# Performance work log

Hardware: AMD Instinct MI355X
Metric: run time of the kernel (lower is better)

Reference implementation:

```python
import jax, jax.numpy as jnp
import numpy as np

DIM = 768
HEADS = 12
HEAD_DIM = DIM // HEADS
HIDDEN = int(DIM * 4.0)
EPS = 1e-5


def _layernorm(x, g, b):
    mu = jnp.mean(x, axis=-1, keepdims=True)
    var = jnp.mean(jnp.square(x - mu), axis=-1, keepdims=True)
    return (x - mu) * jax.lax.rsqrt(var + EPS) * g + b


def setup_inputs() -> dict:
    key = jax.random.key(0)
    ks = jax.random.split(key, 8)
    s_in = 1.0 / np.sqrt(DIM)
    s_hid = 1.0 / np.sqrt(HIDDEN)
    return {
        "x": jax.random.normal(ks[0], (2, 2048, DIM), dtype=jnp.float32),
        "ln1_g": jnp.ones((DIM,), jnp.float32),
        "ln1_b": jnp.zeros((DIM,), jnp.float32),
        "w_qkv": jax.random.normal(ks[1], (DIM, 3 * DIM), jnp.float32) * s_in,
        "w_proj": jax.random.normal(ks[2], (DIM, DIM), jnp.float32) * s_in,
        "b_proj": jnp.zeros((DIM,), jnp.float32),
        "ln2_g": jnp.ones((DIM,), jnp.float32),
        "ln2_b": jnp.zeros((DIM,), jnp.float32),
        "w_fc1": jax.random.normal(ks[3], (DIM, HIDDEN), jnp.float32) * s_in,
        "b_fc1": jnp.zeros((HIDDEN,), jnp.float32),
        "w_fc2": jax.random.normal(ks[4], (HIDDEN, DIM), jnp.float32) * s_hid,
        "b_fc2": jnp.zeros((DIM,), jnp.float32),
    }


def reference(x, ln1_g, ln1_b, w_qkv, w_proj, b_proj, ln2_g, ln2_b, w_fc1, b_fc1, w_fc2, b_fc2):
    b, n, c = x.shape
    scale = HEAD_DIM ** -0.5

    # --- attention branch ---
    h = _layernorm(x, ln1_g, ln1_b)
    qkv = (h @ w_qkv).reshape(b, n, 3, HEADS, HEAD_DIM)
    q, k, v = jnp.moveaxis(qkv, 2, 0)          # each [b, n, H, hd]
    attn = jnp.einsum("bqhd,bkhd->bhqk", q, k) * scale
    attn = jax.nn.softmax(attn, axis=-1)       # [b, H, n, n] (naive, materialized)
    o = jnp.einsum("bhqk,bkhd->bqhd", attn, v).reshape(b, n, c)
    x = x + o @ w_proj + b_proj

    # --- MLP branch ---
    h2 = _layernorm(x, ln2_g, ln2_b)
    m = jax.nn.gelu(h2 @ w_fc1 + b_fc1, approximate=False)
    x = x + m @ w_fc2 + b_fc2
    return x
```

## Files before the change

### kernel.cpp

```cpp
#include <hip/hip_runtime.h>
#include <math.h>


typedef unsigned short u16;
typedef __attribute__((ext_vector_type(8))) short short8;
typedef __attribute__((ext_vector_type(4))) float f32x4;

#define TOKENS 4096
#define DIM    768
#define QKV_N  2304
#define HID    3072
#define NSEQ   2048
#define NHEAD  12
#define HDIM   64

__device__ __forceinline__ float bf2f(u16 u) {
  union { unsigned i; float f; } v; v.i = ((unsigned)u) << 16; return v.f;
}
__device__ __forceinline__ u16 f2bf(float f) {
  union { float f; unsigned i; } v; v.f = f;
  unsigned r = v.i + 0x7fffu + ((v.i >> 16) & 1u);
  return (u16)(r >> 16);
}
__device__ __forceinline__ unsigned pack_bf2(float a, float b) {
  union { float f; unsigned i; } x, y; x.f = a; y.f = b;
  return (x.i >> 16) | (y.i & 0xffff0000u);
}
__device__ __forceinline__ void pl32swap(unsigned &a, unsigned &b) {
  asm("v_permlane32_swap_b32 %0, %1" : "+v"(a), "+v"(b));
}
__device__ __forceinline__ void pl16swap(unsigned &a, unsigned &b) {
  asm("v_permlane16_swap_b32 %0, %1" : "+v"(a), "+v"(b));
}

__device__ __forceinline__ void async_copy16(const u16* g, u16* l) {
  __builtin_amdgcn_global_load_lds(
      (const __attribute__((address_space(1))) unsigned int*)(unsigned long long)g,
      (__attribute__((address_space(3))) unsigned int*)(unsigned int)(unsigned long long)l,
      16, 0, 0);
}

__global__ __launch_bounds__(256) void prep_kernel(
    const float* __restrict__ x, const float* __restrict__ g,
    const float* __restrict__ b, u16* __restrict__ h,
    const float* __restrict__ in0, u16* __restrict__ out0,
    const float* __restrict__ in1, u16* __restrict__ out1,
    const float* __restrict__ in2, u16* __restrict__ out2,
    const float* __restrict__ in3, u16* __restrict__ out3) {
  const int tid = threadIdx.x;
  if (blockIdx.x < 1024) {
    int wave = tid >> 6, lane = tid & 63;
    int token = blockIdx.x * 4 + wave;
    float v[12];
    const float4* xr = (const float4*)(x + (size_t)token * DIM);
#pragma unroll
    for (int w = 0; w < 3; w++) {
      float4 q = xr[lane + w * 64];
      v[w * 4 + 0] = q.x; v[w * 4 + 1] = q.y; v[w * 4 + 2] = q.z; v[w * 4 + 3] = q.w;
    }
    float s = 0.f;
#pragma unroll
    for (int i = 0; i < 12; i++) s += v[i];
#pragma unroll
    for (int off = 32; off > 0; off >>= 1) s += __shfl_xor(s, off);
    float mu = s * (1.0f / DIM);
    float ss = 0.f;
#pragma unroll
    for (int i = 0; i < 12; i++) { float d = v[i] - mu; ss += d * d; }
#pragma unroll
    for (int off = 32; off > 0; off >>= 1) ss += __shfl_xor(ss, off);
    float rs = rsqrtf(ss * (1.0f / DIM) + 1e-5f);
    ushort4* orow = (ushort4*)(h + (size_t)token * DIM);
    const float4* g4 = (const float4*)g;
    const float4* b4 = (const float4*)b;
#pragma unroll
    for (int w = 0; w < 3; w++) {
      float4 gq = g4[lane + w * 64], bq = b4[lane + w * 64];
      ushort4 o;
      o.x = f2bf((v[w * 4 + 0] - mu) * rs * gq.x + bq.x);
      o.y = f2bf((v[w * 4 + 1] - mu) * rs * gq.y + bq.y);
      o.z = f2bf((v[w * 4 + 2] - mu) * rs * gq.z + bq.z);
      o.w = f2bf((v[w * 4 + 3] - mu) * rs * gq.w + bq.w);
      orow[lane + w * 64] = o;
    }
    return;
  }
  __shared__ u16 t[32][33];
  int bid = blockIdx.x - 1024, rem;
  const float* in; u16* out; int R, C;
  if (bid < 1728)      { in = in0; out = out0; R = 768;  C = 2304; rem = bid; }
  else if (bid < 2304) { in = in1; out = out1; R = 768;  C = 768;  rem = bid - 1728; }
  else if (bid < 4608) { in = in2; out = out2; R = 768;  C = 3072; rem = bid - 2304; }
  else                 { in = in3; out = out3; R = 3072; C = 768;  rem = bid - 4608; }
  int c0 = (rem % (C / 32)) * 32, r0 = (rem / (C / 32)) * 32;
  int tx = tid & 31, ty = tid >> 5;
#pragma unroll
  for (int i = 0; i < 4; i++)
    t[ty + i * 8][tx] = f2bf(in[(size_t)(r0 + ty + i * 8) * C + c0 + tx]);
  __syncthreads();
#pragma unroll
  for (int i = 0; i < 4; i++)
    out[(size_t)(c0 + ty + i * 8) * R + r0 + tx] = t[tx][ty + i * 8];
}

__global__ __launch_bounds__(256) void ln_kernel(const u16* __restrict__ xin,
                                                 const float* __restrict__ g,
                                                 const float* __restrict__ b,
                                                 u16* __restrict__ out) {
  int wave = threadIdx.x >> 6, lane = threadIdx.x & 63;
  int token = blockIdx.x * 4 + wave;
  float v[12];
  const ushort4* xr = (const ushort4*)(xin + (size_t)token * DIM);
#pragma unroll
  for (int w = 0; w < 3; w++) {
    ushort4 q = xr[lane + w * 64];
    v[w * 4 + 0] = bf2f(q.x); v[w * 4 + 1] = bf2f(q.y);
    v[w * 4 + 2] = bf2f(q.z); v[w * 4 + 3] = bf2f(q.w);
  }
  float s = 0.f;
#pragma unroll
  for (int i = 0; i < 12; i++) s += v[i];
#pragma unroll
  for (int off = 32; off > 0; off >>= 1) s += __shfl_xor(s, off);
  float mu = s * (1.0f / DIM);
  float ss = 0.f;
#pragma unroll
  for (int i = 0; i < 12; i++) { float d = v[i] - mu; ss += d * d; }
#pragma unroll
  for (int off = 32; off > 0; off >>= 1) ss += __shfl_xor(ss, off);
  float rs = rsqrtf(ss * (1.0f / DIM) + 1e-5f);

  ushort4* orow = (ushort4*)(out + (size_t)token * DIM);
  const float4* g4 = (const float4*)g;
  const float4* b4 = (const float4*)b;
#pragma unroll
  for (int w = 0; w < 3; w++) {
    float4 gq = g4[lane + w * 64], bq = b4[lane + w * 64];
    ushort4 o;
    o.x = f2bf((v[w * 4 + 0] - mu) * rs * gq.x + bq.x);
    o.y = f2bf((v[w * 4 + 1] - mu) * rs * gq.y + bq.y);
    o.z = f2bf((v[w * 4 + 2] - mu) * rs * gq.z + bq.z);
    o.w = f2bf((v[w * 4 + 3] - mu) * rs * gq.w + bq.w);
    orow[lane + w * 64] = o;
  }
}

template <int BM, int BN, int EPI>
__global__ __launch_bounds__(256, 3) void gemm_bt(
    const u16* __restrict__ A, const u16* __restrict__ BT,
    void* __restrict__ Cout, const float* __restrict__ bias,
    const void* __restrict__ resid, int M, int N, int K,
    u16* __restrict__ vtb) {
  constexpr int MT = BM / 32, NT = BN / 32;
  constexpr int ACH = BM / 16;
  constexpr int CPW = (BM + BN) / 64;
  __shared__ __align__(16) u16 Alds[2][BM * 32];
  __shared__ __align__(16) u16 Blds[2][BN * 32];
  const int tid = threadIdx.x;
  const int lane = tid & 63, wave = tid >> 6;
  const int wr = wave >> 1, wc = wave & 1;
  const int nby = M / BM;
  const int by = blockIdx.x % nby, bx = blockIdx.x / nby;
  const int bm = by * BM, bn = bx * BN;
  const int c16 = lane & 15, quad = lane >> 4;
  const int l4 = lane >> 2;
  const int lc = (((lane & 3) ^ ((l4 >> 1) & 3)) * 8);
  const int fsw = (c16 >> 1) & 3;

  f32x4 acc[MT][NT];
#pragma unroll
  for (int i = 0; i < MT; i++)
#pragma unroll
    for (int j = 0; j < NT; j++) acc[i][j] = (f32x4){0.f, 0.f, 0.f, 0.f};

  const u16* gsrc[CPW];
  u16* ldst[CPW];
  int hstep[CPW];
#pragma unroll
  for (int c = 0; c < CPW; c++) {
    int chunk = wave * CPW + c;
    if (chunk < ACH) {
      gsrc[c] = A + (size_t)(bm + chunk * 16 + l4) * K + lc;
      ldst[c] = Alds[0] + chunk * 512;
      hstep[c] = BM * 32;
    } else {
      int bc = chunk - ACH;
      gsrc[c] = BT + (size_t)(bn + bc * 16 + l4) * K + lc;
      ldst[c] = Blds[0] + bc * 512;
      hstep[c] = BN * 32;
    }
  }

  for (int kk = 0; kk < K; kk += 64) {
    __syncthreads();
#pragma unroll
    for (int c = 0; c < CPW; c++) {
      async_copy16(gsrc[c] + kk, ldst[c]);
      async_copy16(gsrc[c] + kk + 32, ldst[c] + hstep[c]);
    }
    __syncthreads();
#pragma unroll
    for (int ks = 0; ks < 2; ks++) {
      short8 af[MT], bfr[NT];
#pragma unroll
      for (int mt = 0; mt < MT; mt++)
        af[mt] = *(const short8*)(Alds[ks] + (wr * (BM / 2) + mt * 16 + c16) * 32 +
                                  ((quad ^ fsw)) * 8);
#pragma unroll
      for (int nt = 0; nt < NT; nt++)
        bfr[nt] = *(const short8*)(Blds[ks] + (wc * (BN / 2) + nt * 16 + c16) * 32 +
                                   ((quad ^ fsw)) * 8);
#pragma unroll
      for (int mt = 0; mt < MT; mt++)
#pragma unroll
        for (int nt = 0; nt < NT; nt++)
          acc[mt][nt] = __builtin_amdgcn_mfma_f32_16x16x32_bf16(af[mt], bfr[nt],
                                                                acc[mt][nt], 0, 0, 0);
    }
  }

#pragma unroll
  for (int mt = 0; mt < MT; mt++) {
#pragma unroll
    for (int nt = 0; nt < NT; nt++) {
      int col = bn + wc * (BN / 2) + nt * 16 + c16;
      float bv = (EPI != 0) ? bias[col] : 0.f;
      int row0 = bm + wr * (BM / 2) + mt * 16 + quad * 4;
      if (EPI == 0 && col >= 2 * DIM) {
        int b = row0 >> 11;
        ushort4 pk;
        pk.x = f2bf(acc[mt][nt][0]); pk.y = f2bf(acc[mt][nt][1]);
        pk.z = f2bf(acc[mt][nt][2]); pk.w = f2bf(acc[mt][nt][3]);
        *(ushort4*)(vtb + ((size_t)b * DIM + col - 2 * DIM) * NSEQ + (row0 & 2047)) = pk;
        continue;
      }
#pragma unroll
      for (int r = 0; r < 4; r++) {
        int row = row0 + r;
        float vv = acc[mt][nt][r];
        if (EPI == 1) {
          vv += bv + ((const float*)resid)[(size_t)row * N + col];
          ((u16*)Cout)[(size_t)row * N + col] = f2bf(vv);
        } else if (EPI == 2) {
          vv += bv;
          vv = 0.5f * vv * (1.0f + erff(vv * 0.70710678118654752f));
          ((u16*)Cout)[(size_t)row * N + col] = f2bf(vv);
        } else if (EPI == 3) {
          vv += bv + bf2f(((const u16*)resid)[(size_t)row * N + col]);
          ((float*)Cout)[(size_t)row * N + col] = vv;
        } else {
          ((u16*)Cout)[(size_t)row * N + col] = f2bf(vv);
        }
      }
    }
  }
}

__global__ __launch_bounds__(256, 3) void attn_kernel(const u16* __restrict__ qkv,
                                                      const u16* __restrict__ vt,
                                                      u16* __restrict__ o) {
  const int tid = threadIdx.x;
  const int lane = tid & 63, wave = tid >> 6;
  const int c16 = lane & 15, quad = lane >> 4;
  const int wq = wave >> 1, wk = wave & 1;
  const int bh = blockIdx.x % (2 * NHEAD);
  const int qt = blockIdx.x / (2 * NHEAD);
  const int bb = bh / NHEAD, h = bh % NHEAD;
  __shared__ __align__(16) u16 Klds[2][64 * 64];
  __shared__ __align__(16) u16 Vtlds[2][64 * 64];
  const size_t base = (size_t)bb * NSEQ * QKV_N;
  const int q0 = qt * 64;
  const int sw = c16 & 7;

  short8 qf[2][2];
#pragma unroll
  for (int qs = 0; qs < 2; qs++) {
    const u16* qp = qkv + base + (size_t)(q0 + wq * 32 + qs * 16 + c16) * QKV_N + h * HDIM;
    qf[qs][0] = *(const short8*)(qp + quad * 8);
    qf[qs][1] = *(const short8*)(qp + 32 + quad * 8);
  }

  float Ls[2] = {0.f, 0.f};
  f32x4 Of[2][4];
#pragma unroll
  for (int qs = 0; qs < 2; qs++)
#pragma unroll
    for (int dt = 0; dt < 4; dt++) Of[qs][dt] = (f32x4){0.f, 0.f, 0.f, 0.f};

  const int srow = lane >> 3;
  const int schunk = (lane & 7) ^ srow;
  const int r0 = wave * 16;
  const u16* ksrc = qkv + base + (size_t)(r0 + srow) * QKV_N + DIM + h * HDIM + schunk * 8;
  const u16* vsrc = vt + ((size_t)bh * HDIM + r0 + srow) * NSEQ + schunk * 8;
  const float SC = 0.18033688011112042f;

#pragma unroll
  for (int j = 0; j < 2; j++) {
    async_copy16(ksrc + (size_t)(8 * j) * QKV_N, Klds[0] + r0 * 64 + 8 * j * 64);
    async_copy16(vsrc + (size_t)(8 * j) * NSEQ, Vtlds[0] + r0 * 64 + 8 * j * 64);
  }

  for (int it = 0; it < NSEQ / 64; it++) {
    const int cur = it & 1;
    __syncthreads();
    if (it + 1 < NSEQ / 64) {
      const int kt1 = (it + 1) * 64;
      u16* kd = Klds[cur ^ 1] + r0 * 64;
      u16* vd = Vtlds[cur ^ 1] + r0 * 64;
#pragma unroll
      for (int j = 0; j < 2; j++) {
        async_copy16(ksrc + (size_t)(kt1 + 8 * j) * QKV_N, kd + 8 * j * 64);
        async_copy16(vsrc + (size_t)(8 * j) * NSEQ + kt1, vd + 8 * j * 64);
      }
    }

    short8 kf0[2], kf1[2];
#pragma unroll
    for (int kt = 0; kt < 2; kt++) {
      const u16* krow = Klds[cur] + (wk * 32 + kt * 16 + c16) * 64;
      kf0[kt] = *(const short8*)(krow + (quad ^ sw) * 8);
      kf1[kt] = *(const short8*)(krow + ((quad + 4) ^ sw) * 8);
    }

    f32x4 St[2][2];
#pragma unroll
    for (int qs = 0; qs < 2; qs++)
#pragma unroll
      for (int kt = 0; kt < 2; kt++) {
        f32x4 s = (f32x4){0.f, 0.f, 0.f, 0.f};
        s = __builtin_amdgcn_mfma_f32_16x16x32_bf16(kf0[kt], qf[qs][0], s, 0, 0, 0);
        s = __builtin_amdgcn_mfma_f32_16x16x32_bf16(kf1[kt], qf[qs][1], s, 0, 0, 0);
        St[qs][kt] = s;
      }

    short8 vf[4];
#pragma unroll
    for (int dt = 0; dt < 4; dt++) {
      const u16* vrow = Vtlds[cur] + (dt * 16 + c16) * 64;
      vf[dt] = *(const short8*)(vrow + ((wk * 4 + quad) ^ sw) * 8);
    }

    short8 pf[2];
#pragma unroll
    for (int qs = 0; qs < 2; qs++) {
      float p[2][4];
#pragma unroll
      for (int kt = 0; kt < 2; kt++)
#pragma unroll
        for (int r = 0; r < 4; r++)
          p[kt][r] = __builtin_amdgcn_exp2f(St[qs][kt][r] * SC);
      Ls[qs] += ((p[0][0] + p[0][1]) + (p[0][2] + p[0][3])) +
                ((p[1][0] + p[1][1]) + (p[1][2] + p[1][3]));
      unsigned a0 = pack_bf2(p[0][0], p[0][1]);
      unsigned a1 = pack_bf2(p[0][2], p[0][3]);
      unsigned b0 = pack_bf2(p[1][0], p[1][1]);
      unsigned b1 = pack_bf2(p[1][2], p[1][3]);
      pl32swap(a0, b0);
      pl32swap(a1, b1);
      pl16swap(a0, b0);
      pl16swap(a1, b1);
      union { unsigned u[4]; short8 s; } pk_;
      pk_.u[0] = a0; pk_.u[1] = a1; pk_.u[2] = b0; pk_.u[3] = b1;
      pf[qs] = pk_.s;
    }

#pragma unroll
    for (int dt = 0; dt < 4; dt++)
#pragma unroll
      for (int qs = 0; qs < 2; qs++)
        Of[qs][dt] = __builtin_amdgcn_mfma_f32_16x16x32_bf16(pf[qs], vf[dt],
                                                             Of[qs][dt], 0, 0, 0);
  }

  __syncthreads();
  float* red = (float*)&Klds[0][0];
  float* lred = (float*)&Vtlds[0][0];
  if (wk == 1) {
    float* dst = red + wq * 2048;
#pragma unroll
    for (int qs = 0; qs < 2; qs++)
#pragma unroll
      for (int dt = 0; dt < 4; dt++)
        *(f32x4*)(dst + (qs * 4 + dt) * 256 + lane * 4) = Of[qs][dt];
    lred[wq * 128 + lane] = Ls[0];
    lred[wq * 128 + 64 + lane] = Ls[1];
  }
  __syncthreads();
  if (wk == 0) {
    const float* src = red + wq * 2048;
#pragma unroll
    for (int qs = 0; qs < 2; qs++)
#pragma unroll
      for (int dt = 0; dt < 4; dt++)
        Of[qs][dt] += *(const f32x4*)(src + (qs * 4 + dt) * 256 + lane * 4);
    float t0 = Ls[0] + lred[wq * 128 + lane];
    float t1 = Ls[1] + lred[wq * 128 + 64 + lane];
    t0 += __shfl_xor(t0, 16); t0 += __shfl_xor(t0, 32);
    t1 += __shfl_xor(t1, 16); t1 += __shfl_xor(t1, 32);
#pragma unroll
    for (int qs = 0; qs < 2; qs++) {
      float tq = qs ? t1 : t0;
#pragma unroll
      for (int r = 0; r < 4; r++) {
        float L = __shfl(tq, quad * 4 + r);
        int token = q0 + wq * 32 + qs * 16 + quad * 4 + r;
        u16* orow = o + (size_t)(bb * NSEQ + token) * DIM + h * HDIM;
#pragma unroll
        for (int dt = 0; dt < 4; dt++)
          orow[dt * 16 + c16] = f2bf(Of[qs][dt][r] / L);
      }
    }
  }
}

extern "C" void kernel_launch(void* const* d_in, const int* in_sizes, int n_in,
                              void* d_out, int out_size, void* d_ws, size_t ws_size,
                              hipStream_t stream) {
  (void)in_sizes; (void)n_in; (void)out_size; (void)ws_size;
  const float* x      = (const float*)d_in[0];
  const float* ln1_g  = (const float*)d_in[1];
  const float* ln1_b  = (const float*)d_in[2];
  const float* w_qkv  = (const float*)d_in[3];
  const float* w_proj = (const float*)d_in[4];
  const float* b_proj = (const float*)d_in[5];
  const float* ln2_g  = (const float*)d_in[6];
  const float* ln2_b  = (const float*)d_in[7];
  const float* w_fc1  = (const float*)d_in[8];
  const float* b_fc1  = (const float*)d_in[9];
  const float* w_fc2  = (const float*)d_in[10];
  const float* b_fc2  = (const float*)d_in[11];
  float* out = (float*)d_out;

  char* p = (char*)d_ws;
  u16* h_bf   = (u16*)p; p += (size_t)TOKENS * DIM * 2;
  u16* qkv_bf = (u16*)p; p += (size_t)TOKENS * QKV_N * 2;
  u16* o_bf   = (u16*)p; p += (size_t)TOKENS * DIM * 2;
  u16* x1_bf  = (u16*)p; p += (size_t)TOKENS * DIM * 2;
  u16* wprojT = (u16*)p; p += (size_t)DIM * DIM * 2;
  u16* wfc1T  = (u16*)p; p += (size_t)HID * DIM * 2;
  u16* wfc2T  = (u16*)p; p += (size_t)DIM * HID * 2;
  u16* wqkvT  = (u16*)p; p += (size_t)QKV_N * DIM * 2;
  u16* vtb    = (u16*)p; p += (size_t)TOKENS * DIM * 2;
  u16* m_bf   = qkv_bf;

  prep_kernel<<<dim3(1024 + 6912), 256, 0, stream>>>(
      x, ln1_g, ln1_b, h_bf,
      w_qkv, wqkvT, w_proj, wprojT, w_fc1, wfc1T, w_fc2, wfc2T);

  gemm_bt<64, 128, 0><<<dim3((QKV_N / 128) * (TOKENS / 64)), 256, 0, stream>>>(
      h_bf, wqkvT, qkv_bf, nullptr, nullptr, TOKENS, QKV_N, DIM, vtb);
  attn_kernel<<<dim3(2 * NHEAD * (NSEQ / 64)), 256, 0, stream>>>(qkv_bf, vtb, o_bf);
  gemm_bt<64, 64, 1><<<dim3((DIM / 64) * (TOKENS / 64)), 256, 0, stream>>>(
      o_bf, wprojT, x1_bf, b_proj, x, TOKENS, DIM, DIM, nullptr);
  ln_kernel<<<TOKENS / 4, 256, 0, stream>>>(x1_bf, ln2_g, ln2_b, h_bf);
  gemm_bt<128, 128, 2><<<dim3((HID / 128) * (TOKENS / 128)), 256, 0, stream>>>(
      h_bf, wfc1T, m_bf, b_fc1, nullptr, TOKENS, HID, DIM, nullptr);
  gemm_bt<64, 64, 3><<<dim3((DIM / 64) * (TOKENS / 64)), 256, 0, stream>>>(
      m_bf, wfc2T, out, b_fc2, x1_bf, TOKENS, DIM, HID, nullptr);
}
```

Baseline: 250.7 us.

## Load K/V fragments directly from global in attention, drop LDS staging

The attention kernel no longer stages K and V^T tiles through double-buffered LDS with async copies and per-iteration barriers. Each wave now loads its MFMA fragments straight from global memory, relying on the L2/L1 caches. It also swaps the truncating bf16 pack for the hardware v_cvt_pk_bf16_f32 conversion (round-to-nearest) and raises wave priority around the MFMA blocks. This removes __syncthreads and the LDS traffic, at the cost of redundant global loads across waves and exposed global-load latency with no explicit prefetch.

```diff
diff --git a/kernel.cpp b/kernel.cpp
--- a/kernel.cpp
+++ b/kernel.cpp
@@ -22,9 +22,10 @@
   unsigned r = v.i + 0x7fffu + ((v.i >> 16) & 1u);
   return (u16)(r >> 16);
 }
-__device__ __forceinline__ unsigned pack_bf2(float a, float b) {
-  union { float f; unsigned i; } x, y; x.f = a; y.f = b;
-  return (x.i >> 16) | (y.i & 0xffff0000u);
+__device__ __forceinline__ unsigned cvt_pk_bf16(float lo, float hi) {
+  unsigned r;
+  asm("v_cvt_pk_bf16_f32 %0, %1, %2" : "=v"(r) : "v"(lo), "v"(hi));
+  return r;
 }
 __device__ __forceinline__ void pl32swap(unsigned &a, unsigned &b) {
   asm("v_permlane32_swap_b32 %0, %1" : "+v"(a), "+v"(b));
@@ -266,11 +267,10 @@
   const int bh = blockIdx.x % (2 * NHEAD);
   const int qt = blockIdx.x / (2 * NHEAD);
   const int bb = bh / NHEAD, h = bh % NHEAD;
-  __shared__ __align__(16) u16 Klds[2][64 * 64];
-  __shared__ __align__(16) u16 Vtlds[2][64 * 64];
+  __shared__ __align__(16) float red[4096];
+  __shared__ float lred[256];
   const size_t base = (size_t)bb * NSEQ * QKV_N;
   const int q0 = qt * 64;
-  const int sw = c16 & 7;
 
   short8 qf[2][2];
 #pragma unroll
@@ -287,42 +287,26 @@
 #pragma unroll
     for (int dt = 0; dt < 4; dt++) Of[qs][dt] = (f32x4){0.f, 0.f, 0.f, 0.f};
 
-  const int srow = lane >> 3;
-  const int schunk = (lane & 7) ^ srow;
-  const int r0 = wave * 16;
-  const u16* ksrc = qkv + base + (size_t)(r0 + srow) * QKV_N + DIM + h * HDIM + schunk * 8;
-  const u16* vsrc = vt + ((size_t)bh * HDIM + r0 + srow) * NSEQ + schunk * 8;
+  const u16* kp = qkv + base + (size_t)(wk * 32 + c16) * QKV_N + DIM + h * HDIM + quad * 8;
+  const u16* vp = vt + ((size_t)bh * HDIM + c16) * NSEQ + wk * 32 + quad * 8;
   const float SC = 0.18033688011112042f;
 
-#pragma unroll
-  for (int j = 0; j < 2; j++) {
-    async_copy16(ksrc + (size_t)(8 * j) * QKV_N, Klds[0] + r0 * 64 + 8 * j * 64);
-    async_copy16(vsrc + (size_t)(8 * j) * NSEQ, Vtlds[0] + r0 * 64 + 8 * j * 64);
-  }
-
   for (int it = 0; it < NSEQ / 64; it++) {
-    const int cur = it & 1;
-    __syncthreads();
-    if (it + 1 < NSEQ / 64) {
-      const int kt1 = (it + 1) * 64;
-      u16* kd = Klds[cur ^ 1] + r0 * 64;
-      u16* vd = Vtlds[cur ^ 1] + r0 * 64;
-#pragma unroll
-      for (int j = 0; j < 2; j++) {
-        async_copy16(ksrc + (size_t)(kt1 + 8 * j) * QKV_N, kd + 8 * j * 64);
-        async_copy16(vsrc + (size_t)(8 * j) * NSEQ + kt1, vd + 8 * j * 64);
-      }
-    }
-
+    const u16* kb = kp + (size_t)it * 64 * QKV_N;
     short8 kf0[2], kf1[2];
 #pragma unroll
     for (int kt = 0; kt < 2; kt++) {
-      const u16* krow = Klds[cur] + (wk * 32 + kt * 16 + c16) * 64;
-      kf0[kt] = *(const short8*)(krow + (quad ^ sw) * 8);
-      kf1[kt] = *(const short8*)(krow + ((quad + 4) ^ sw) * 8);
-    }
+      kf0[kt] = *(const short8*)(kb + (size_t)kt * 16 * QKV_N);
+      kf1[kt] = *(const short8*)(kb + (size_t)kt * 16 * QKV_N + 32);
+    }
+    const u16* vb = vp + it * 64;
+    short8 vf[4];
+#pragma unroll
+    for (int dt = 0; dt < 4; dt++)
+      vf[dt] = *(const short8*)(vb + (size_t)dt * 16 * NSEQ);
 
     f32x4 St[2][2];
+    __builtin_amdgcn_s_setprio(1);
 #pragma unroll
     for (int qs = 0; qs < 2; qs++)
 #pragma unroll
@@ -332,13 +316,7 @@
         s = __builtin_amdgcn_mfma_f32_16x16x32_bf16(kf1[kt], qf[qs][1], s, 0, 0, 0);
         St[qs][kt] = s;
       }
-
-    short8 vf[4];
-#pragma unroll
-    for (int dt = 0; dt < 4; dt++) {
-      const u16* vrow = Vtlds[cur] + (dt * 16 + c16) * 64;
-      vf[dt] = *(const short8*)(vrow + ((wk * 4 + quad) ^ sw) * 8);
-    }
+    __builtin_amdgcn_s_setprio(0);
 
     short8 pf[2];
 #pragma unroll
@@ -351,10 +329,10 @@
           p[kt][r] = __builtin_amdgcn_exp2f(St[qs][kt][r] * SC);
       Ls[qs] += ((p[0][0] + p[0][1]) + (p[0][2] + p[0][3])) +
                 ((p[1][0] + p[1][1]) + (p[1][2] + p[1][3]));
-      unsigned a0 = pack_bf2(p[0][0], p[0][1]);
-      unsigned a1 = pack_bf2(p[0][2], p[0][3]);
-      unsigned b0 = pack_bf2(p[1][0], p[1][1]);
-      unsigned b1 = pack_bf2(p[1][2], p[1][3]);
+      unsigned a0 = cvt_pk_bf16(p[0][0], p[0][1]);
+      unsigned a1 = cvt_pk_bf16(p[0][2], p[0][3]);
+      unsigned b0 = cvt_pk_bf16(p[1][0], p[1][1]);
+      unsigned b1 = cvt_pk_bf16(p[1][2], p[1][3]);
       pl32swap(a0, b0);
       pl32swap(a1, b1);
       pl16swap(a0, b0);
@@ -364,17 +342,16 @@
       pf[qs] = pk_.s;
     }
 
+    __builtin_amdgcn_s_setprio(1);
 #pragma unroll
     for (int dt = 0; dt < 4; dt++)
 #pragma unroll
       for (int qs = 0; qs < 2; qs++)
         Of[qs][dt] = __builtin_amdgcn_mfma_f32_16x16x32_bf16(pf[qs], vf[dt],
                                                              Of[qs][dt], 0, 0, 0);
-  }
-
-  __syncthreads();
-  float* red = (float*)&Klds[0][0];
-  float* lred = (float*)&Vtlds[0][0];
+    __builtin_amdgcn_s_setprio(0);
+  }
+
   if (wk == 1) {
     float* dst = red + wq * 2048;
 #pragma unroll
```

Measured after the change: 306.5 us. 1.22x slower.
